# Kernel tuning notes

Hardware: AMD Instinct MI355X
Metric: run time of the kernel (lower is better)

## Reference

```python
import jax, jax.numpy as jnp
import numpy as np

B, D, L = 2, 1024, 4096   # batch, channels (= num_heads), seq len
FS = 4                    # filter_size
DEPTH = 11                # ceil(log2((L-1)/(FS-1)+1))
LN_EPS = 1e-5


def setup_inputs() -> dict:
    key = jax.random.key(0)
    ks = jax.random.split(key, 7)
    return {
        "x": jax.random.normal(ks[0], (B, D, L), jnp.float32),
        "h0": jax.random.normal(ks[1], (D, 1, FS), jnp.float32) * 0.2,
        "h1": jax.random.normal(ks[2], (D, 1, FS), jnp.float32) * 0.2,
        "w_mix": jax.random.normal(ks[3], (D, D), jnp.float32) / np.sqrt(D),
        "b_mix": jnp.zeros((D,), jnp.float32),
        "ln_gamma": jnp.ones((D,), jnp.float32),
        "ln_beta": jnp.zeros((D,), jnp.float32),
    }


def _dw_conv(a, h, dilation):
    # depthwise (groups = D) dilated conv1d, cross-correlation like torch
    return jax.lax.conv_general_dilated(
        a, h, window_strides=(1,), padding='VALID',
        rhs_dilation=(dilation,),
        dimension_numbers=('NCH', 'OIH', 'NCH'),
        feature_group_count=D)


def reference(x, h0, h1, w_mix, b_mix, ln_gamma, ln_beta):
    # --- multires conv tree ---
    a = x
    dilation = 1
    a_list, b_list = [], []
    for _ in range(DEPTH):
        pad = dilation * (FS - 1)
        ap = jnp.pad(a, ((0, 0), (0, 0), (pad, 0)))  # left causal pad
        b = _dw_conv(ap, h1, dilation)
        a = _dw_conv(ap, h0, dilation)
        a_list.append(a)
        b_list.append(b)
        dilation *= 2
    # --- gated combination across scales (deepest level first) ---
    a_rev = a_list[::-1]
    b_rev = b_list[::-1]
    y = jnp.zeros_like(x)
    gated = None
    for i in range(DEPTH):
        if i + 1 < DEPTH:
            gated = jax.nn.sigmoid(a_rev[i]) * b_rev[i + 1]
        # last iteration reuses the previous gated tensor (matches original)
        y = y + gated
    # --- 1x1 channel mix (Dropout1d is identity in eval) + residual ---
    mixed = jnp.einsum('oc,bcl->bol', w_mix, y) + b_mix[None, :, None]
    z = mixed + x
    # --- LayerNorm over channel dim ---
    mu = jnp.mean(z, axis=1, keepdims=True)
    var = jnp.mean(jnp.square(z - mu), axis=1, keepdims=True)
    out = (z - mu) * jax.lax.rsqrt(var + LN_EPS)
    out = out * ln_gamma[None, :, None] + ln_beta[None, :, None]
    return out
```

## Files before the change

### kernel.cpp

```cpp
#include <hip/hip_runtime.h>
#include <hip/hip_bf16.h>

#define NB 2
#define ND 1024
#define NL 4096
#define NFS 4
#define NDEPTH 11
#define LN_EPS 1e-5f

#define BM 128
#define BN 128
#define BK 32
#define NKI (ND / BK)
#define ASZ (BM * BK)

#define CPAD 3072
#define CBUF (CPAD + NL)

typedef __bf16 bf16x8 __attribute__((ext_vector_type(8)));
typedef float f32x4 __attribute__((ext_vector_type(4)));
typedef _Float16 half8 __attribute__((ext_vector_type(8)));

__device__ __forceinline__ unsigned short f2bf(float f) {
    __hip_bfloat16 h = __float2bfloat16(f);
    unsigned short u;
    __builtin_memcpy(&u, &h, 2);
    return u;
}

__device__ __forceinline__ float bf2f(unsigned short u) {
    unsigned int ui = (unsigned int)u << 16;
    float f;
    __builtin_memcpy(&f, &ui, 4);
    return f;
}

__device__ __forceinline__ unsigned int pack2bf(float lo, float hi) {
    return (unsigned int)f2bf(lo) | ((unsigned int)f2bf(hi) << 16);
}

__device__ __forceinline__ float sigm(float v) {
    return __builtin_amdgcn_rcpf(1.f + __expf(-v));
}

__device__ __forceinline__ void llds16(const void* g, void* l) {
    __builtin_amdgcn_global_load_lds(
        (const __attribute__((address_space(1))) unsigned int*)g,
        (__attribute__((address_space(3))) unsigned int*)l, 16, 0, 0);
}

__global__ __launch_bounds__(256) void wconv_kernel(const float* __restrict__ w,
                                                    unsigned short* __restrict__ wbf) {
    const int idx8 = (blockIdx.x * 256 + threadIdx.x) * 8;
    const float4 v0 = *reinterpret_cast<const float4*>(w + idx8);
    const float4 v1 = *reinterpret_cast<const float4*>(w + idx8 + 4);
    uint4 o;
    o.x = pack2bf(v0.x, v0.y);
    o.y = pack2bf(v0.z, v0.w);
    o.z = pack2bf(v1.x, v1.y);
    o.w = pack2bf(v1.z, v1.w);
    *reinterpret_cast<uint4*>(wbf + idx8) = o;
}

__global__ __launch_bounds__(512, 8) void conv_cascade_kernel(const float* __restrict__ x,
                                                              const float* __restrict__ h0,
                                                              const float* __restrict__ h1,
                                                              unsigned short* __restrict__ ybf) {
    __shared__ _Float16 a_sh[CBUF];
    const int row = blockIdx.x;
    const int d = row & (ND - 1);
    const int t = threadIdx.x;

    if (t < CPAD / 8) *reinterpret_cast<half8*>(&a_sh[t * 8]) = (half8)0;

    const float* xrow = x + (size_t)row * NL;

    _Float16 h0c[NFS], h1c[NFS];
#pragma unroll
    for (int k = 0; k < NFS; ++k) {
        h0c[k] = (_Float16)h0[d * NFS + k];
        h1c[k] = (_Float16)h1[d * NFS + k];
    }

    half8 cur;
    {
        const float4 v0 = *reinterpret_cast<const float4*>(xrow + t * 8);
        const float4 v1 = *reinterpret_cast<const float4*>(xrow + t * 8 + 4);
        cur[0] = (_Float16)v0.x; cur[1] = (_Float16)v0.y;
        cur[2] = (_Float16)v0.z; cur[3] = (_Float16)v0.w;
        cur[4] = (_Float16)v1.x; cur[5] = (_Float16)v1.y;
        cur[6] = (_Float16)v1.z; cur[7] = (_Float16)v1.w;
    }
    const int A = CPAD + t * 8;
    *reinterpret_cast<half8*>(&a_sh[A]) = cur;

    float yacc[8];
    half8 bprev = (half8)0;
#pragma unroll
    for (int j = 0; j < 8; ++j) yacc[j] = 0.f;
    __syncthreads();

    half8 an, bn;

#define CONV_MATH(a1, a2, a3)                                       \
    an = cur * h0c[3] + (a1)*h0c[2] + (a2)*h0c[1] + (a3)*h0c[0];    \
    bn = cur * h1c[3] + (a1)*h1c[2] + (a2)*h1c[1] + (a3)*h1c[0];

#define CONV_FIN(SC)                                                \
    {                                                               \
        *reinterpret_cast<half8*>(&a_sh[A]) = an;                   \
        if ((SC) > 0.f) {                                           \
            _Pragma("unroll") for (int j = 0; j < 8; ++j)           \
                yacc[j] += (SC)*sigm((float)an[j]) * (float)bprev[j]; \
        }                                                           \
        cur = an;                                                   \
        bprev = bn;                                                 \
    }

    {
        const half8 m = *reinterpret_cast<const half8*>(&a_sh[A - 8]);
        const half8 a1 = __builtin_shufflevector(m, cur, 7, 8, 9, 10, 11, 12, 13, 14);
        const half8 a2 = __builtin_shufflevector(m, cur, 6, 7, 8, 9, 10, 11, 12, 13);
        const half8 a3 = __builtin_shufflevector(m, cur, 5, 6, 7, 8, 9, 10, 11, 12);
        CONV_MATH(a1, a2, a3)
        __syncthreads();
        CONV_FIN(0.f)
        __syncthreads();
    }

    {
        const half8 m = *reinterpret_cast<const half8*>(&a_sh[A - 8]);
        const half8 a1 = __builtin_shufflevector(m, cur, 6, 7, 8, 9, 10, 11, 12, 13);
        const half8 a2 = __builtin_shufflevector(m, cur, 4, 5, 6, 7, 8, 9, 10, 11);
        const half8 a3 = __builtin_shufflevector(m, cur, 2, 3, 4, 5, 6, 7, 8, 9);
        CONV_MATH(a1, a2, a3)
        __syncthreads();
        CONV_FIN(2.f)
        __syncthreads();
    }

    {
        const half8 m = *reinterpret_cast<const half8*>(&a_sh[A - 8]);
        const half8 m2 = *reinterpret_cast<const half8*>(&a_sh[A - 16]);
        const half8 a1 = __builtin_shufflevector(m, cur, 4, 5, 6, 7, 8, 9, 10, 11);
        const half8 a2 = m;
        const half8 a3 = __builtin_shufflevector(m2, m, 4, 5, 6, 7, 8, 9, 10, 11);
        CONV_MATH(a1, a2, a3)
        __syncthreads();
        CONV_FIN(1.f)
        __syncthreads();
    }

    int dil = 8;
#pragma unroll 1
    for (int lev = 3; lev <= 9; ++lev) {
        const half8 a1 = *reinterpret_cast<const half8*>(&a_sh[A - dil]);
        const half8 a2 = *reinterpret_cast<const half8*>(&a_sh[A - 2 * dil]);
        const half8 a3 = *reinterpret_cast<const half8*>(&a_sh[A - 3 * dil]);
        CONV_MATH(a1, a2, a3)
        __syncthreads();
        CONV_FIN(1.f)
        dil <<= 1;
        __syncthreads();
    }

    {
        const half8 a1 = *reinterpret_cast<const half8*>(&a_sh[A - 1024]);
        const half8 a2 = *reinterpret_cast<const half8*>(&a_sh[A - 2048]);
        const half8 a3 = *reinterpret_cast<const half8*>(&a_sh[A - 3072]);
        an = cur * h0c[3] + a1 * h0c[2] + a2 * h0c[1] + a3 * h0c[0];
#pragma unroll
        for (int j = 0; j < 8; ++j)
            yacc[j] += sigm((float)an[j]) * (float)bprev[j];
    }
#undef CONV_MATH
#undef CONV_FIN

    uint4 o;
    o.x = pack2bf(yacc[0], yacc[1]);
    o.y = pack2bf(yacc[2], yacc[3]);
    o.z = pack2bf(yacc[4], yacc[5]);
    o.w = pack2bf(yacc[6], yacc[7]);
    *reinterpret_cast<uint4*>(ybf + (size_t)row * NL + t * 8) = o;
}

__global__ __launch_bounds__(256) void transpose_kernel(const unsigned short* __restrict__ ybf,
                                                        unsigned short* __restrict__ yT) {
    __shared__ unsigned short tile[64][66];
    const int l0 = blockIdx.x * 64;
    const int c0 = blockIdx.y * 64;
    const int b = blockIdx.z;
    const int t = threadIdx.x;
    const int li = t & 63, cg = t >> 6;
#pragma unroll
    for (int k = 0; k < 16; ++k) {
        const int ci = cg * 16 + k;
        tile[ci][li] = ybf[(size_t)(b * ND + c0 + ci) * NL + l0 + li];
    }
    __syncthreads();
    const int ci2 = t & 63, lg = t >> 6;
#pragma unroll
    for (int k = 0; k < 16; ++k) {
        const int li2 = lg * 16 + k;
        yT[((size_t)b * NL + l0 + li2) * ND + c0 + ci2] = tile[ci2][li2];
    }
}

__global__ __launch_bounds__(256) void gemm_kernel(const unsigned short* __restrict__ wbf,
                                                   const unsigned short* __restrict__ yT,
                                                   const float* __restrict__ bmix,
                                                   unsigned short* __restrict__ mixed) {
    __shared__ unsigned short As[3][BM][BK];
    __shared__ unsigned short Bs[3][BN][BK];

    const int n0 = blockIdx.x * BN;
    const int m0 = blockIdx.y * BM;
    const int b = blockIdx.z;
    const int t = threadIdx.x;
    const int lane = t & 63, wid = t >> 6;
    const int wr = wid >> 1, wc = wid & 1;
    const int fr = lane & 15;
    const int fk = (lane >> 4) * 8;

    const int srow = wid * 32 + (lane >> 2);
    const int sk = (lane & 3) * 8;
    const unsigned short* Ag = wbf + (size_t)(m0 + srow) * ND + sk;
    const unsigned short* Bg = yT + ((size_t)b * NL + n0 + srow) * ND + sk;
    unsigned short* A0 = &As[0][0][0];
    unsigned short* B0 = &Bs[0][0][0];
    unsigned short* AsW = A0 + wid * 32 * BK;
    unsigned short* BsW = B0 + wid * 32 * BK;

#define STAGE(bo, kt)                           \
    llds16(Ag + (kt), AsW + (bo));              \
    llds16(Ag + (kt) + 16 * ND, AsW + (bo) + 16 * BK); \
    llds16(Bg + (kt), BsW + (bo));              \
    llds16(Bg + (kt) + 16 * ND, BsW + (bo) + 16 * BK);

    f32x4 acc[4][4];
#pragma unroll
    for (int mi = 0; mi < 4; ++mi)
#pragma unroll
        for (int ni = 0; ni < 4; ++ni)
            acc[mi][ni] = (f32x4){0.f, 0.f, 0.f, 0.f};

    STAGE(0, 0)
    STAGE(ASZ, BK)

    int bc = 0;
    int bs = 2;
#pragma unroll 1
    for (int ki = 0; ki < NKI; ++ki) {
        if (ki + 1 < NKI) {
            asm volatile("s_waitcnt vmcnt(4)" ::: "memory");
        } else {
            asm volatile("s_waitcnt vmcnt(0)" ::: "memory");
        }
        __builtin_amdgcn_s_barrier();
        __builtin_amdgcn_sched_barrier(0);

        if (ki + 2 < NKI) {
            const int bo = bs * ASZ;
            const int kt = (ki + 2) * BK;
            STAGE(bo, kt)
        }

        const int bco = bc * ASZ;
        bf16x8 af[4], bv[4];
#pragma unroll
        for (int mi = 0; mi < 4; ++mi)
            af[mi] = *reinterpret_cast<const bf16x8*>(A0 + bco + (wr * 64 + mi * 16 + fr) * BK + fk);
#pragma unroll
        for (int ni = 0; ni < 4; ++ni)
            bv[ni] = *reinterpret_cast<const bf16x8*>(B0 + bco + (wc * 64 + ni * 16 + fr) * BK + fk);
#pragma unroll
        for (int mi = 0; mi < 4; ++mi)
#pragma unroll
            for (int ni = 0; ni < 4; ++ni)
                acc[mi][ni] = __builtin_amdgcn_mfma_f32_16x16x32_bf16(af[mi], bv[ni],
                                                                      acc[mi][ni], 0, 0, 0);
        bc = (bc == 2) ? 0 : bc + 1;
        bs = (bs == 2) ? 0 : bs + 1;
    }
#undef STAGE

    const size_t bbase = (size_t)b * ND * NL;
#pragma unroll
    for (int mi = 0; mi < 4; ++mi) {
#pragma unroll
        for (int r = 0; r < 4; ++r) {
            const int o = m0 + wr * 64 + mi * 16 + (lane >> 4) * 4 + r;
            const float bm = bmix[o];
            const size_t rowbase = bbase + (size_t)o * NL;
#pragma unroll
            for (int ni = 0; ni < 4; ++ni) {
                const int l = n0 + wc * 64 + ni * 16 + fr;
                mixed[rowbase + l] = f2bf(acc[mi][ni][r] + bm);
            }
        }
    }
}

__global__ __launch_bounds__(512) void ln_kernel(const unsigned short* __restrict__ mixed,
                                                 const float* __restrict__ x,
                                                 const float* __restrict__ gamma,
                                                 const float* __restrict__ beta,
                                                 float* __restrict__ out) {
    const int b = blockIdx.y;
    const int l0 = blockIdx.x * 32;
    const int tl = threadIdx.x & 31, tg = threadIdx.x >> 5;
    const size_t base = (size_t)b * ND * NL + l0 + tl;

    float zv[64];
    float s = 0.f, q = 0.f;
#pragma unroll
    for (int j = 0; j < 64; ++j) {
        const size_t idx = base + (size_t)(tg + j * 16) * NL;
        const float v = bf2f(mixed[idx]) + x[idx];
        zv[j] = v;
        s += v;
        q += v * v;
    }

    __shared__ float sred[16][33], qred[16][33];
    __shared__ float mu_s[32], rs_s[32];
    sred[tg][tl] = s;
    qred[tg][tl] = q;
    __syncthreads();
    if (tg == 0) {
        float S = 0.f, Q = 0.f;
#pragma unroll
        for (int g = 0; g < 16; ++g) {
            S += sred[g][tl];
            Q += qred[g][tl];
        }
        const float mu = S * (1.f / ND);
        const float var = Q * (1.f / ND) - mu * mu;
        mu_s[tl] = mu;
        rs_s[tl] = rsqrtf(var + LN_EPS);
    }
    __syncthreads();
    const float mu = mu_s[tl], rs = rs_s[tl];
#pragma unroll
    for (int j = 0; j < 64; ++j) {
        const int c = tg + j * 16;
        out[base + (size_t)c * NL] = (zv[j] - mu) * rs * gamma[c] + beta[c];
    }
}

extern "C" void kernel_launch(void* const* d_in, const int* in_sizes, int n_in,
                              void* d_out, int out_size, void* d_ws, size_t ws_size,
                              hipStream_t stream) {
    (void)in_sizes; (void)n_in; (void)out_size; (void)ws_size;
    const float* x = (const float*)d_in[0];
    const float* h0 = (const float*)d_in[1];
    const float* h1 = (const float*)d_in[2];
    const float* wmix = (const float*)d_in[3];
    const float* bmix = (const float*)d_in[4];
    const float* gamma = (const float*)d_in[5];
    const float* beta = (const float*)d_in[6];
    float* out = (float*)d_out;

    char* ws = (char*)d_ws;
    unsigned short* ybf = (unsigned short*)(ws);
    unsigned short* yT = (unsigned short*)(ws + (size_t)16 * 1024 * 1024);
    unsigned short* wbf = (unsigned short*)(ws + (size_t)32 * 1024 * 1024);
    unsigned short* mixed = (unsigned short*)(ws + (size_t)34 * 1024 * 1024);

    wconv_kernel<<<dim3(ND * ND / (256 * 8)), 256, 0, stream>>>(wmix, wbf);
    conv_cascade_kernel<<<dim3(NB * ND), 512, 0, stream>>>(x, h0, h1, ybf);
    transpose_kernel<<<dim3(NL / 64, ND / 64, NB), 256, 0, stream>>>(ybf, yT);
    gemm_kernel<<<dim3(NL / BN, ND / BM, NB), 256, 0, stream>>>(wbf, yT, bmix, mixed);
    ln_kernel<<<dim3(NL / 32, NB), 512, 0, stream>>>(mixed, x, gamma, beta, out);
}
```

Baseline: 105.2 us.

## Double-buffer conv cascade LDS, fp16 packed gating, remap GEMM blocks for XCD locality

The conv cascade now ping-pongs between two LDS buffers, so each level needs one barrier instead of two. The sigmoid-gate accumulation moves from fp32 to packed half2 math using exp2 and rcp. The GEMM launches a 1D grid and remaps block IDs so blocks sharing the same weight and activation tiles are grouped per XCD for cache reuse. Risks are lower accuracy from accumulating y in fp16 and doubled LDS use per block, which may lower occupancy.

Result: faster. 99.98 us (-5.0%).

```diff
diff --git a/kernel.cpp b/kernel.cpp
--- a/kernel.cpp
+++ b/kernel.cpp
@@ -1,5 +1,6 @@
 #include <hip/hip_runtime.h>
 #include <hip/hip_bf16.h>
+#include <hip/hip_fp16.h>
 
 #define NB 2
 #define ND 1024
@@ -37,10 +38,6 @@
 
 __device__ __forceinline__ unsigned int pack2bf(float lo, float hi) {
     return (unsigned int)f2bf(lo) | ((unsigned int)f2bf(hi) << 16);
-}
-
-__device__ __forceinline__ float sigm(float v) {
-    return __builtin_amdgcn_rcpf(1.f + __expf(-v));
 }
 
 __device__ __forceinline__ void llds16(const void* g, void* l) {
@@ -66,12 +63,15 @@
                                                               const float* __restrict__ h0,
                                                               const float* __restrict__ h1,
                                                               unsigned short* __restrict__ ybf) {
-    __shared__ _Float16 a_sh[CBUF];
+    __shared__ _Float16 a_sh[2][CBUF];
     const int row = blockIdx.x;
     const int d = row & (ND - 1);
     const int t = threadIdx.x;
 
-    if (t < CPAD / 8) *reinterpret_cast<half8*>(&a_sh[t * 8]) = (half8)0;
+    if (t < CPAD / 8) {
+        *reinterpret_cast<half8*>(&a_sh[0][t * 8]) = (half8)0;
+        *reinterpret_cast<half8*>(&a_sh[1][t * 8]) = (half8)0;
+    }
 
     const float* xrow = x + (size_t)row * NL;
 
@@ -82,6 +82,7 @@
         h1c[k] = (_Float16)h1[d * NFS + k];
     }
 
+    const int A = CPAD + t * 8;
     half8 cur;
     {
         const float4 v0 = *reinterpret_cast<const float4*>(xrow + t * 8);
@@ -91,96 +92,111 @@
         cur[4] = (_Float16)v1.x; cur[5] = (_Float16)v1.y;
         cur[6] = (_Float16)v1.z; cur[7] = (_Float16)v1.w;
     }
-    const int A = CPAD + t * 8;
-    *reinterpret_cast<half8*>(&a_sh[A]) = cur;
-
-    float yacc[8];
+    _Float16* rbp = &a_sh[0][0];
+    _Float16* wbp = &a_sh[1][0];
+    *reinterpret_cast<half8*>(&rbp[A]) = cur;
+
+    const __half2 nlog2e = __float2half2_rn(-1.44269504f);
+    const __half2 one2 = __float2half2_rn(1.f);
+    const __half2 two2 = __float2half2_rn(2.f);
+    __half2 yacc2[4];
+#pragma unroll
+    for (int p = 0; p < 4; ++p) yacc2[p] = __float2half2_rn(0.f);
     half8 bprev = (half8)0;
-#pragma unroll
-    for (int j = 0; j < 8; ++j) yacc[j] = 0.f;
     __syncthreads();
 
     half8 an, bn;
 
-#define CONV_MATH(a1, a2, a3)                                       \
+#define CMATH(a1, a2, a3)                                           \
     an = cur * h0c[3] + (a1)*h0c[2] + (a2)*h0c[1] + (a3)*h0c[0];    \
     bn = cur * h1c[3] + (a1)*h1c[2] + (a2)*h1c[1] + (a3)*h1c[0];
 
-#define CONV_FIN(SC)                                                \
+#define GATE(SC2)                                                   \
     {                                                               \
-        *reinterpret_cast<half8*>(&a_sh[A]) = an;                   \
-        if ((SC) > 0.f) {                                           \
-            _Pragma("unroll") for (int j = 0; j < 8; ++j)           \
-                yacc[j] += (SC)*sigm((float)an[j]) * (float)bprev[j]; \
+        __half2 ap[4], bp[4];                                       \
+        __builtin_memcpy(ap, &an, 16);                              \
+        __builtin_memcpy(bp, &bprev, 16);                           \
+        _Pragma("unroll") for (int p = 0; p < 4; ++p) {             \
+            const __half2 e = h2exp2(__hmul2(ap[p], nlog2e));       \
+            const __half2 s = h2rcp(__hadd2(e, one2));              \
+            const __half2 g = __hmul2(__hmul2(s, bp[p]), SC2);      \
+            yacc2[p] = __hadd2(g, yacc2[p]);                        \
         }                                                           \
+    }
+
+#define CFIN()                                                      \
+    {                                                               \
+        *reinterpret_cast<half8*>(&wbp[A]) = an;                    \
         cur = an;                                                   \
         bprev = bn;                                                 \
-    }
-
-    {
-        const half8 m = *reinterpret_cast<const half8*>(&a_sh[A - 8]);
+        _Float16* tmpp = rbp; rbp = wbp; wbp = tmpp;                \
+    }
+
+    {
+        const half8 m = *reinterpret_cast<const half8*>(&rbp[A - 8]);
         const half8 a1 = __builtin_shufflevector(m, cur, 7, 8, 9, 10, 11, 12, 13, 14);
         const half8 a2 = __builtin_shufflevector(m, cur, 6, 7, 8, 9, 10, 11, 12, 13);
         const half8 a3 = __builtin_shufflevector(m, cur, 5, 6, 7, 8, 9, 10, 11, 12);
-        CONV_MATH(a1, a2, a3)
+        CMATH(a1, a2, a3)
+        CFIN()
         __syncthreads();
-        CONV_FIN(0.f)
-        __syncthreads();
-    }
-
-    {
-        const half8 m = *reinterpret_cast<const half8*>(&a_sh[A - 8]);
+    }
+
+    {
+        const half8 m = *reinterpret_cast<const half8*>(&rbp[A - 8]);
         const half8 a1 = __builtin_shufflevector(m, cur, 6, 7, 8, 9, 10, 11, 12, 13);
         const half8 a2 = __builtin_shufflevector(m, cur, 4, 5, 6, 7, 8, 9, 10, 11);
         const half8 a3 = __builtin_shufflevector(m, cur, 2, 3, 4, 5, 6, 7, 8, 9);
-        CONV_MATH(a1, a2, a3)
+        CMATH(a1, a2, a3)
+        GATE(two2)
+        CFIN()
         __syncthreads();
-        CONV_FIN(2.f)
-        __syncthreads();
-    }
-
-    {
-        const half8 m = *reinterpret_cast<const half8*>(&a_sh[A - 8]);
-        const half8 m2 = *reinterpret_cast<const half8*>(&a_sh[A - 16]);
+    }
+
+    {
+        const half8 m = *reinterpret_cast<const half8*>(&rbp[A - 8]);
+        const half8 m2 = *reinterpret_cast<const half8*>(&rbp[A - 16]);
         const half8 a1 = __builtin_shufflevector(m, cur, 4, 5, 6, 7, 8, 9, 10, 11);
-        const half8 a2 = m;
         const half8 a3 = __builtin_shufflevector(m2, m, 4, 5, 6, 7, 8, 9, 10, 11);
-        CONV_MATH(a1, a2, a3)
-        __syncthreads();
-        CONV_FIN(1.f)
+        CMATH(a1, m, a3)
+        GATE(one2)
+        CFIN()
         __syncthreads();
     }
 
     int dil = 8;
 #pragma unroll 1
     for (int lev = 3; lev <= 9; ++lev) {
-        const half8 a1 = *reinterpret_cast<const half8*>(&a_sh[A - dil]);
-        const half8 a2 = *reinterpret_cast<const half8*>(&a_sh[A - 2 * dil]);
-        const half8 a3 = *reinterpret_cast<const half8*>(&a_sh[A - 3 * dil]);
-        CONV_MATH(a1, a2, a3)
-        __syncthreads();
-        CONV_FIN(1.f)
+        const half8 a1 = *reinterpret_cast<const half8*>(&rbp[A - dil]);
+        const half8 a2 = *reinterpret_cast<const half8*>(&rbp[A - 2 * dil]);
+        const half8 a3 = *reinterpret_cast<const half8*>(&rbp[A - 3 * dil]);
+        CMATH(a1, a2, a3)
+        GATE(one2)
+        CFIN()
         dil <<= 1;
         __syncthreads();
     }
 
     {
-        const half8 a1 = *reinterpret_cast<const half8*>(&a_sh[A - 1024]);
-        const half8 a2 = *reinterpret_cast<const half8*>(&a_sh[A - 2048]);
-        const half8 a3 = *reinterpret_cast<const half8*>(&a_sh[A - 3072]);
+        const half8 a1 = *reinterpret_cast<const half8*>(&rbp[A - 1024]);
+        const half8 a2 = *reinterpret_cast<const half8*>(&rbp[A - 2048]);
+        const half8 a3 = *reinterpret_cast<const half8*>(&rbp[A - 3072]);
         an = cur * h0c[3] + a1 * h0c[2] + a2 * h0c[1] + a3 * h0c[0];
-#pragma unroll
-        for (int j = 0; j < 8; ++j)
-            yacc[j] += sigm((float)an[j]) * (float)bprev[j];
-    }
-#undef CONV_MATH
-#undef CONV_FIN
-
+        GATE(one2)
+    }
+#undef CMATH
+#undef GATE
+#undef CFIN
+
+    const float2 f0 = __half22float2(yacc2[0]);
+    const float2 f1 = __half22float2(yacc2[1]);
+    const float2 f2 = __half22float2(yacc2[2]);
+    const float2 f3 = __half22float2(yacc2[3]);
     uint4 o;
-    o.x = pack2bf(yacc[0], yacc[1]);
-    o.y = pack2bf(yacc[2], yacc[3]);
-    o.z = pack2bf(yacc[4], yacc[5]);
-    o.w = pack2bf(yacc[6], yacc[7]);
+    o.x = pack2bf(f0.x, f0.y);
+    o.y = pack2bf(f1.x, f1.y);
+    o.z = pack2bf(f2.x, f2.y);
+    o.w = pack2bf(f3.x, f3.y);
     *reinterpret_cast<uint4*>(ybf + (size_t)row * NL + t * 8) = o;
 }
 
@@ -213,9 +229,12 @@
     __shared__ unsigned short As[3][BM][BK];
     __shared__ unsigned short Bs[3][BN][BK];
 
-    const int n0 = blockIdx.x * BN;
-    const int m0 = blockIdx.y * BM;
-    const int b = blockIdx.z;
+    const int orig = blockIdx.x;
+    const int wgid = (orig & 7) * 64 + (orig >> 3);
+    const int b = wgid & 1;
+    const int m0 = ((wgid >> 1) & 7) * BM;
+    const int n0 = (wgid >> 4) * BN;
+
     const int t = threadIdx.x;
     const int lane = t & 63, wid = t >> 6;
     const int wr = wid >> 1, wc = wid & 1;
@@ -370,6 +389,6 @@
     wconv_kernel<<<dim3(ND * ND / (256 * 8)), 256, 0, stream>>>(wmix, wbf);
     conv_cascade_kernel<<<dim3(NB * ND), 512, 0, stream>>>(x, h0, h1, ybf);
     transpose_kernel<<<dim3(NL / 64, ND / 64, NB), 256, 0, stream>>>(ybf, yT);
-    gemm_kernel<<<dim3(NL / BN, ND / BM, NB), 256, 0, stream>>>(wbf, yT, bmix, mixed);
+    gemm_kernel<<<dim3(512), 256, 0, stream>>>(wbf, yT, bmix, mixed);
     ln_kernel<<<dim3(NL / 32, NB), 512, 0, stream>>>(mixed, x, gamma, beta, out);
 }
```
